# Optimization experiments

Hardware: AMD Instinct MI355X
Metric: run time of the kernel (lower is better)

Reference implementation:

```python
import jax, jax.numpy as jnp
import numpy as np

B, S, D = 2, 2048, 2048
H, DP = 16, 128
WINDOW = 512


def setup_inputs() -> dict:
    key = jax.random.key(0)
    ks = jax.random.split(key, 9)
    sc = 0.02
    return {
        "x": jax.random.normal(ks[0], (B, S, D), dtype=jnp.float32),
        "wq": jax.random.normal(ks[1], (D, H * DP), dtype=jnp.float32) * sc,
        "bq": jax.random.normal(ks[2], (H * DP,), dtype=jnp.float32) * sc,
        "wk": jax.random.normal(ks[3], (D, H * DP), dtype=jnp.float32) * sc,
        "bk": jax.random.normal(ks[4], (H * DP,), dtype=jnp.float32) * sc,
        "wv": jax.random.normal(ks[5], (D, H * DP), dtype=jnp.float32) * sc,
        "bv": jax.random.normal(ks[6], (H * DP,), dtype=jnp.float32) * sc,
        "wo": jax.random.normal(ks[7], (H * DP,), dtype=jnp.float32) * sc,
        "bo": jax.random.normal(ks[8], (1,), dtype=jnp.float32) * sc,
    }


def _sliding_window_mask(seq_len, window):
    q_idx = jnp.arange(seq_len)[:, None]
    kv_idx = jnp.arange(seq_len)[None, :]
    return (q_idx >= kv_idx) & (q_idx - kv_idx < window)


def reference(x, wq, bq, wk, bk, wv, bv, wo, bo):
    b, s, _ = x.shape
    # QKV projections -> (B, H, S, DP)
    q = (x @ wq + bq).reshape(b, s, H, DP).transpose(0, 2, 1, 3)
    k = (x @ wk + bk).reshape(b, s, H, DP).transpose(0, 2, 1, 3)
    v = (x @ wv + bv).reshape(b, s, H, DP).transpose(0, 2, 1, 3)
    scale = 1.0 / np.sqrt(DP).astype(np.float32)
    scores = jnp.einsum("bhqd,bhkd->bhqk", q, k) * scale  # (B,H,S,S)
    mask = _sliding_window_mask(s, WINDOW)
    scores = jnp.where(mask, scores, jnp.finfo(scores.dtype).min)
    attn = jax.nn.softmax(scores, axis=-1)
    o = jnp.einsum("bhqk,bhkd->bhqd", attn, v)  # (B,H,S,DP)
    o = o.transpose(0, 2, 1, 3).reshape(b, s, H * DP)
    return o @ wo + bo[0]  # (B, S)
```

## Files before the change

kernel.cpp:

```cpp
#include <hip/hip_runtime.h>

typedef unsigned short USH;
typedef __bf16 v8bf __attribute__((ext_vector_type(8)));
typedef float v4f __attribute__((ext_vector_type(4)));
typedef unsigned short us8 __attribute__((ext_vector_type(8)));

#define SB 2048
#define DD 2048
#define NH 16
#define DPH 128

__device__ __forceinline__ USH f2bf(float f) {
  unsigned u = __float_as_uint(f);
  u = u + 0x7fffu + ((u >> 16) & 1u);
  return (USH)(u >> 16);
}

#define GL16(gp, lp)                                                   \
  __builtin_amdgcn_global_load_lds(                                    \
      (const __attribute__((address_space(1))) void*)(gp),             \
      (__attribute__((address_space(3))) void*)(lp), 16, 0, 0)

__global__ __launch_bounds__(256) void k_prep(const float* __restrict__ x,
    const float* __restrict__ wq, const float* __restrict__ wk,
    const float* __restrict__ wvf, const float* __restrict__ bvf,
    const float* __restrict__ wo,
    USH* __restrict__ xb, USH* __restrict__ wqt, USH* __restrict__ wkt,
    USH* __restrict__ wvoT, float* __restrict__ bvo, float* __restrict__ out) {
  __shared__ USH tl[64][72];
  __shared__ float red[256];
  const int bid = blockIdx.x;
  const int t = threadIdx.x;
  if (bid < 4096) {
    const int i = (bid * 256 + t) * 8;
    const float4 a = *(const float4*)&x[i];
    const float4 b = *(const float4*)&x[i + 4];
    v8bf o;
    o[0] = (__bf16)a.x; o[1] = (__bf16)a.y; o[2] = (__bf16)a.z; o[3] = (__bf16)a.w;
    o[4] = (__bf16)b.x; o[5] = (__bf16)b.y; o[6] = (__bf16)b.z; o[7] = (__bf16)b.w;
    *(v8bf*)&xb[i] = o;
  } else if (bid < 6144) {
    const int rel = bid - 4096;
    const int z = rel >> 10, rem = rel & 1023;
    const float* w = z ? wk : wq;
    USH* wt = z ? wkt : wqt;
    const int k0 = (rem >> 5) * 64, j0 = (rem & 31) * 64;
#pragma unroll
    for (int p = 0; p < 4; ++p) {
      const int r = p * 16 + (t >> 4);
      const int c = (t & 15) * 4;
      const float4 v = *(const float4*)&w[(size_t)(k0 + r) * DD + j0 + c];
      tl[c + 0][r] = f2bf(v.x);
      tl[c + 1][r] = f2bf(v.y);
      tl[c + 2][r] = f2bf(v.z);
      tl[c + 3][r] = f2bf(v.w);
    }
    __syncthreads();
#pragma unroll
    for (int p = 0; p < 2; ++p) {
      const int j = p * 32 + (t >> 3);
      const int seg = (t & 7) * 8;
      us8 v = *(const us8*)&tl[j][seg];
      *(us8*)&wt[(size_t)(j0 + j) * DD + k0 + seg] = v;
    }
  } else if (bid < 8193) {
    const int d = bid - 6144;
    const float* src = (d == DD) ? bvf : (wvf + (size_t)d * DD);
    const float4 a0 = *(const float4*)&src[t * 8];
    const float4 a1 = *(const float4*)&src[t * 8 + 4];
    const float4 w0 = *(const float4*)&wo[t * 8];
    const float4 w1 = *(const float4*)&wo[t * 8 + 4];
    red[t] = a0.x * w0.x + a0.y * w0.y + a0.z * w0.z + a0.w * w0.w +
             a1.x * w1.x + a1.y * w1.y + a1.z * w1.z + a1.w * w1.w;
    __syncthreads();
    for (int s = 8; s > 0; s >>= 1) {
      if ((t & 15) < s) red[t] += red[t + s];
      __syncthreads();
    }
    if ((t & 15) == 0) {
      if (d == DD) bvo[t >> 4] = red[t];
      else wvoT[(size_t)(t >> 4) * DD + d] = f2bf(red[t]);
    }
  } else {
#pragma unroll
    for (int i = 0; i < 16; ++i) out[i * 256 + t] = 0.f;
  }
}

__global__ __launch_bounds__(64) void k_vw2(const USH* __restrict__ xb,
    const USH* __restrict__ wvoT, const float* __restrict__ bvo,
    float* __restrict__ vw) {
  const int lane = threadIdx.x & 63;
  const int lr = lane & 15, g = lane >> 4;
  const int r0 = blockIdx.x * 16;
  v4f acc = (v4f){0.f, 0.f, 0.f, 0.f};
  const USH* ap = xb + (size_t)(r0 + lr) * DD + g * 8;
  const USH* bp = wvoT + (size_t)lr * DD + g * 8;
#pragma unroll 4
  for (int kt = 0; kt < 64; ++kt) {
    v8bf af = *(const v8bf*)(ap + kt * 32);
    v8bf bf = *(const v8bf*)(bp + kt * 32);
    acc = __builtin_amdgcn_mfma_f32_16x16x32_bf16(af, bf, acc, 0, 0, 0);
  }
  const float bb = bvo[lr];
#pragma unroll
  for (int rr = 0; rr < 4; ++rr) {
    const int row = r0 + g * 4 + rr;
    vw[((size_t)(row >> 11) * NH + lr) * SB + (row & 2047)] = acc[rr] + bb;
  }
}

__global__ __launch_bounds__(512, 2) void k_gemm256(
    const USH* __restrict__ xb,
    const USH* __restrict__ wqt, const USH* __restrict__ wkt,
    const float* __restrict__ bq, const float* __restrict__ bk,
    USH* __restrict__ Qb, USH* __restrict__ Kb) {
  __shared__ USH As[2][16384];
  __shared__ USH Bs[2][16384];
  const int fid = blockIdx.x;
  const int nid = (fid & 7) * 32 + (fid >> 3);
  const int z = nid >> 7;
  const int ty = (nid >> 3) & 15, tx = nid & 7;
  const int row0 = ty * 256, col0 = tx * 256;
  const USH* wt = z ? wkt : wqt;
  const float* bias = z ? bk : bq;
  USH* outp = z ? Kb : Qb;
  const float qscale = z ? 1.0f : 0.08838834764831845f;
  const int t = threadIdx.x;
  const int w = t >> 6, lane = t & 63;
  const int lr = lane & 15, g = lane >> 4;
  const int wr = w >> 2, wc = w & 3;
  size_t gA[4], gB[4];
  int ldsOff[4];
#pragma unroll
  for (int q = 0; q < 4; ++q) {
    const int p = q * 512 + t;
    const int row = p >> 3, ps = p & 7;
    const int sl = ps ^ (row & 7);
    gA[q] = (size_t)(row0 + row) * DD + sl * 8;
    gB[q] = (size_t)(col0 + row) * DD + sl * 8;
    ldsOff[q] = p * 8;
  }
  const int swz = (g ^ (lr & 7)) * 8;
  const int k1o = swz ^ 32;
  const int rowA = wr * 128 + lr;
  const int rowB = wc * 64 + lr;

  v4f acc[8][4];
#pragma unroll
  for (int i = 0; i < 8; ++i)
#pragma unroll
    for (int j = 0; j < 4; ++j) acc[i][j] = (v4f){0.f, 0.f, 0.f, 0.f};

#pragma unroll
  for (int q = 0; q < 4; ++q) {
    GL16(xb + gA[q], &As[0][ldsOff[q]]);
    GL16(wt + gB[q], &Bs[0][ldsOff[q]]);
  }
#pragma unroll
  for (int q = 0; q < 4; ++q) {
    GL16(xb + gA[q] + 64, &As[1][ldsOff[q]]);
    GL16(wt + gB[q] + 64, &Bs[1][ldsOff[q]]);
  }
  asm volatile("s_waitcnt vmcnt(8)" ::: "memory");
  __builtin_amdgcn_s_barrier();
  __builtin_amdgcn_sched_barrier(0);

  v8bf bfr0[4], bfr1[4], af0[4], af4[4], af1[4], af5[4];
#pragma unroll
  for (int ni = 0; ni < 4; ++ni)
    bfr0[ni] = *(const v8bf*)&Bs[0][(rowB + ni * 16) * 64 + swz];
#pragma unroll
  for (int mi = 0; mi < 4; ++mi)
    af0[mi] = *(const v8bf*)&As[0][(rowA + mi * 16) * 64 + swz];

  for (int kt = 0; kt < 32; ++kt) {
    const int c = kt & 1;
    const USH* Ab = &As[c][0];
    const USH* Bb = &Bs[c][0];
    __builtin_amdgcn_sched_barrier(0);
#pragma unroll
    for (int mi = 0; mi < 4; ++mi)
      af4[mi] = *(const v8bf*)&Ab[(rowA + (mi + 4) * 16) * 64 + swz];
    asm volatile("s_waitcnt lgkmcnt(4)" ::: "memory");
    __builtin_amdgcn_sched_barrier(0);
    __builtin_amdgcn_s_setprio(1);
#pragma unroll
    for (int mi = 0; mi < 4; ++mi)
#pragma unroll
      for (int ni = 0; ni < 4; ++ni)
        acc[mi][ni] = __builtin_amdgcn_mfma_f32_16x16x32_bf16(af0[mi], bfr0[ni], acc[mi][ni], 0, 0, 0);
    __builtin_amdgcn_s_setprio(0);
    __builtin_amdgcn_sched_barrier(0);
#pragma unroll
    for (int ni = 0; ni < 4; ++ni)
      bfr1[ni] = *(const v8bf*)&Bb[(rowB + ni * 16) * 64 + k1o];
#pragma unroll
    for (int mi = 0; mi < 4; ++mi)
      af1[mi] = *(const v8bf*)&Ab[(rowA + mi * 16) * 64 + k1o];
    asm volatile("s_waitcnt lgkmcnt(8)" ::: "memory");
    __builtin_amdgcn_sched_barrier(0);
    __builtin_amdgcn_s_setprio(1);
#pragma unroll
    for (int mi = 0; mi < 4; ++mi)
#pragma unroll
      for (int ni = 0; ni < 4; ++ni)
        acc[mi + 4][ni] = __builtin_amdgcn_mfma_f32_16x16x32_bf16(af4[mi], bfr0[ni], acc[mi + 4][ni], 0, 0, 0);
    __builtin_amdgcn_s_setprio(0);
    __builtin_amdgcn_sched_barrier(0);
#pragma unroll
    for (int mi = 0; mi < 4; ++mi)
      af5[mi] = *(const v8bf*)&Ab[(rowA + (mi + 4) * 16) * 64 + k1o];
    asm volatile("s_waitcnt lgkmcnt(4)" ::: "memory");
    __builtin_amdgcn_sched_barrier(0);
    __builtin_amdgcn_s_setprio(1);
#pragma unroll
    for (int mi = 0; mi < 4; ++mi)
#pragma unroll
      for (int ni = 0; ni < 4; ++ni)
        acc[mi][ni] = __builtin_amdgcn_mfma_f32_16x16x32_bf16(af1[mi], bfr1[ni], acc[mi][ni], 0, 0, 0);
    __builtin_amdgcn_s_setprio(0);
    asm volatile("s_waitcnt lgkmcnt(0)" ::: "memory");
    __builtin_amdgcn_sched_barrier(0);
    __builtin_amdgcn_s_barrier();
    if (kt < 30) {
      const size_t ko = (size_t)(kt + 2) * 64;
#pragma unroll
      for (int q = 0; q < 4; ++q) {
        GL16(xb + gA[q] + ko, &As[c][ldsOff[q]]);
        GL16(wt + gB[q] + ko, &Bs[c][ldsOff[q]]);
      }
    }
    __builtin_amdgcn_s_setprio(1);
#pragma unroll
    for (int mi = 0; mi < 4; ++mi)
#pragma unroll
      for (int ni = 0; ni < 4; ++ni)
        acc[mi + 4][ni] = __builtin_amdgcn_mfma_f32_16x16x32_bf16(af5[mi], bfr1[ni], acc[mi + 4][ni], 0, 0, 0);
    __builtin_amdgcn_s_setprio(0);
    if (kt < 31) {
      if (kt < 30) {
        asm volatile("s_waitcnt vmcnt(8)" ::: "memory");
      } else {
        asm volatile("s_waitcnt vmcnt(0)" ::: "memory");
      }
      __builtin_amdgcn_s_barrier();
      __builtin_amdgcn_sched_barrier(0);
      const USH* An = &As[c ^ 1][0];
      const USH* Bn = &Bs[c ^ 1][0];
#pragma unroll
      for (int ni = 0; ni < 4; ++ni)
        bfr0[ni] = *(const v8bf*)&Bn[(rowB + ni * 16) * 64 + swz];
#pragma unroll
      for (int mi = 0; mi < 4; ++mi)
        af0[mi] = *(const v8bf*)&An[(rowA + mi * 16) * 64 + swz];
    }
  }

  {
    const int hh = (col0 + wc * 64) >> 7;
    const int dpb = (wc & 1) * 64;
    float bvv[4];
#pragma unroll
    for (int ni = 0; ni < 4; ++ni)
      bvv[ni] = bias[col0 + wc * 64 + ni * 16 + lr];
#pragma unroll
    for (int mi = 0; mi < 8; ++mi) {
#pragma unroll
      for (int rr = 0; rr < 4; ++rr) {
        const int row = row0 + wr * 128 + mi * 16 + g * 4 + rr;
        const int bi = row >> 11, s = row & 2047;
        USH* op = &outp[(((size_t)bi * NH + hh) * SB + s) * DPH + dpb + lr];
        op[0]  = f2bf((acc[mi][0][rr] + bvv[0]) * qscale);
        op[16] = f2bf((acc[mi][1][rr] + bvv[1]) * qscale);
        op[32] = f2bf((acc[mi][2][rr] + bvv[2]) * qscale);
        op[48] = f2bf((acc[mi][3][rr] + bvv[3]) * qscale);
      }
    }
  }
}

__global__ __launch_bounds__(512) void k_attn(const USH* __restrict__ Qb,
    const USH* __restrict__ Kb, const float* __restrict__ vw,
    const float* __restrict__ bo, float* __restrict__ out) {
  __shared__ USH Ks[2][8192];
  const int bh = blockIdx.y;
  const int t = threadIdx.x;
  const int wid = t >> 6, lane = t & 63;
  const int lr = lane & 15, g = lane >> 4;
  const int qblk = blockIdx.x * 128;
  const int qb = qblk + wid * 16;
  const USH* Qp = Qb + (size_t)bh * SB * DPH;
  const USH* Kp = Kb + (size_t)bh * SB * DPH;
  const float* vwp = vw + (size_t)bh * SB;

  v8bf qf[4];
  {
    const USH* qrp = Qp + (size_t)(qb + lr) * DPH + g * 8;
#pragma unroll
    for (int kc = 0; kc < 4; ++kc) qf[kc] = *(const v8bf*)(qrp + kc * 32);
  }
  size_t srcO[2];
  int ldsO[2];
#pragma unroll
  for (int q = 0; q < 2; ++q) {
    const int r = t >> 3, ps = t & 7;
    srcO[q] = (size_t)r * DPH + q * 64 + (size_t)(((ps ^ (r & 7)) * 8));
    ldsO[q] = (q * 512 + t) * 8;
  }

  float ls[4], os[4];
#pragma unroll
  for (int r = 0; r < 4; ++r) { ls[r] = 0.f; os[r] = 0.f; }

  const int kb0 = qblk > 511 ? qblk - 512 : 0;
  const int kbend = qblk + 64;

  GL16(Kp + (size_t)kb0 * DPH + srcO[0], &Ks[0][ldsO[0]]);
  GL16(Kp + (size_t)kb0 * DPH + srcO[1], &Ks[0][ldsO[1]]);
  __syncthreads();

  int buf = 0;
  for (int kb = kb0; kb <= kbend; kb += 64, buf ^= 1) {
    if (kb < kbend) {
      GL16(Kp + (size_t)(kb + 64) * DPH + srcO[0], &Ks[buf ^ 1][ldsO[0]]);
      GL16(Kp + (size_t)(kb + 64) * DPH + srcO[1], &Ks[buf ^ 1][ldsO[1]]);
    }
    const USH* base = &Ks[buf][0];
    v4f acc[4];
    float vv[4];
#pragma unroll
    for (int i = 0; i < 4; ++i) {
      v4f a = (v4f){0.f, 0.f, 0.f, 0.f};
#pragma unroll
      for (int kc = 0; kc < 4; ++kc) {
        const int lrow = (kc >> 1) * 64 + i * 16 + lr;
        v8bf kf = *(const v8bf*)&base[lrow * 64 + ((((kc & 1) * 4 + g) ^ (lr & 7)) * 8)];
        a = __builtin_amdgcn_mfma_f32_16x16x32_bf16(qf[kc], kf, a, 0, 0, 0);
      }
      acc[i] = a;
      vv[i] = vwp[kb + i * 16 + lr];
    }
#pragma unroll
    for (int r = 0; r < 4; ++r) {
      const int q_i = qb + g * 4 + r;
      const int k0i = kb + lr;
      float sc0 = acc[0][r], sc1 = acc[1][r], sc2 = acc[2][r], sc3 = acc[3][r];
      sc0 = (k0i <= q_i && q_i - k0i < 512) ? sc0 : -1e30f;
      sc1 = (k0i + 16 <= q_i && q_i - (k0i + 16) < 512) ? sc1 : -1e30f;
      sc2 = (k0i + 32 <= q_i && q_i - (k0i + 32) < 512) ? sc2 : -1e30f;
      sc3 = (k0i + 48 <= q_i && q_i - (k0i + 48) < 512) ? sc3 : -1e30f;
      const float p0 = __expf(sc0);
      const float p1 = __expf(sc1);
      const float p2 = __expf(sc2);
      const float p3 = __expf(sc3);
      ls[r] += (p0 + p1) + (p2 + p3);
      os[r] += (p0 * vv[0] + p1 * vv[1]) + (p2 * vv[2] + p3 * vv[3]);
    }
    __syncthreads();
  }
#pragma unroll
  for (int r = 0; r < 4; ++r) {
    os[r] += __shfl_xor(os[r], 1); ls[r] += __shfl_xor(ls[r], 1);
    os[r] += __shfl_xor(os[r], 2); ls[r] += __shfl_xor(ls[r], 2);
    os[r] += __shfl_xor(os[r], 4); ls[r] += __shfl_xor(ls[r], 4);
    os[r] += __shfl_xor(os[r], 8); ls[r] += __shfl_xor(ls[r], 8);
  }
  if (lr == 0) {
    const float bo16 = bo[0] * 0.0625f;
#pragma unroll
    for (int r = 0; r < 4; ++r)
      atomicAdd(&out[(size_t)(bh >> 4) * SB + qb + g * 4 + r], os[r] / ls[r] + bo16);
  }
}

extern "C" void kernel_launch(void* const* d_in, const int* in_sizes, int n_in,
                              void* d_out, int out_size, void* d_ws, size_t ws_size,
                              hipStream_t stream) {
  const float* x   = (const float*)d_in[0];
  const float* wq  = (const float*)d_in[1];
  const float* bq  = (const float*)d_in[2];
  const float* wk  = (const float*)d_in[3];
  const float* bk  = (const float*)d_in[4];
  const float* wvf = (const float*)d_in[5];
  const float* bvf = (const float*)d_in[6];
  const float* wo  = (const float*)d_in[7];
  const float* bo  = (const float*)d_in[8];
  float* out = (float*)d_out;
  char* ws = (char*)d_ws;

  USH*   wqt = (USH*)(ws);
  USH*   wkt = (USH*)(ws + 8388608);
  USH*   Qb  = (USH*)(ws + 16777216);
  USH*   Kb  = (USH*)(ws + 33554432);
  float* vw  = (float*)(ws + 50331648);
  USH*   wvoT= (USH*)(ws + 50593792);
  float* bvo = (float*)(ws + 50724864);
  USH*   xbf = (USH*)(ws + 50987264);

  k_prep<<<dim3(8194), dim3(256), 0, stream>>>(x, wq, wk, wvf, bvf, wo,
                                               xbf, wqt, wkt, wvoT, bvo, out);
  k_vw2<<<dim3(256), dim3(64), 0, stream>>>(xbf, wvoT, bvo, vw);
  k_gemm256<<<dim3(256), dim3(512), 0, stream>>>(xbf, wqt, wkt, bq, bk, Qb, Kb);
  k_attn<<<dim3(16, 32), dim3(512), 0, stream>>>(Qb, Kb, vw, bo, out);
}
```

Measured before the change: 117.0 us.

## Replace 256x256 QK projection GEMM with simpler 128x128 tiled kernel

The Q/K projection GEMM moves from 256x256 tiles with 512 threads and a hand-scheduled, interleaved LDS/MFMA pipeline to 128x128 tiles with 256 threads and a plain double-buffered loop. The launch grows from 256 to 1024 blocks, which gives more blocks per CU and better CU fill. In exchange, each tile reuses its operands less, so more global and LDS traffic is needed per FLOP. It also loses the fine-grained waitcnt and sched_barrier overlap and waits on all loads every iteration.

```diff
diff --git a/kernel.cpp b/kernel.cpp
--- a/kernel.cpp
+++ b/kernel.cpp
@@ -110,18 +110,19 @@
   }
 }
 
-__global__ __launch_bounds__(512, 2) void k_gemm256(
+__global__ __launch_bounds__(256, 2) void k_gemm128(
     const USH* __restrict__ xb,
     const USH* __restrict__ wqt, const USH* __restrict__ wkt,
     const float* __restrict__ bq, const float* __restrict__ bk,
     USH* __restrict__ Qb, USH* __restrict__ Kb) {
-  __shared__ USH As[2][16384];
-  __shared__ USH Bs[2][16384];
+  __shared__ USH As[2][8192];
+  __shared__ USH Bs[2][8192];
   const int fid = blockIdx.x;
-  const int nid = (fid & 7) * 32 + (fid >> 3);
-  const int z = nid >> 7;
-  const int ty = (nid >> 3) & 15, tx = nid & 7;
-  const int row0 = ty * 256, col0 = tx * 256;
+  const int swzid = (fid & 7) * 128 + (fid >> 3);
+  const int z = swzid >> 9;
+  const int rem = swzid & 511;
+  const int ty = rem >> 4, tx = rem & 15;
+  const int row0 = ty * 128, col0 = tx * 128;
   const USH* wt = z ? wkt : wqt;
   const float* bias = z ? bk : bq;
   USH* outp = z ? Kb : Qb;
@@ -129,12 +130,12 @@
   const int t = threadIdx.x;
   const int w = t >> 6, lane = t & 63;
   const int lr = lane & 15, g = lane >> 4;
-  const int wr = w >> 2, wc = w & 3;
+  const int wr = w >> 1, wc = w & 1;
   size_t gA[4], gB[4];
   int ldsOff[4];
 #pragma unroll
   for (int q = 0; q < 4; ++q) {
-    const int p = q * 512 + t;
+    const int p = q * 256 + t;
     const int row = p >> 3, ps = p & 7;
     const int sl = ps ^ (row & 7);
     gA[q] = (size_t)(row0 + row) * DD + sl * 8;
@@ -142,13 +143,12 @@
     ldsOff[q] = p * 8;
   }
   const int swz = (g ^ (lr & 7)) * 8;
-  const int k1o = swz ^ 32;
-  const int rowA = wr * 128 + lr;
+  const int rowA = wr * 64 + lr;
   const int rowB = wc * 64 + lr;
 
-  v4f acc[8][4];
-#pragma unroll
-  for (int i = 0; i < 8; ++i)
+  v4f acc[4][4];
+#pragma unroll
+  for (int i = 0; i < 4; ++i)
 #pragma unroll
     for (int j = 0; j < 4; ++j) acc[i][j] = (v4f){0.f, 0.f, 0.f, 0.f};
 
@@ -157,118 +157,53 @@
     GL16(xb + gA[q], &As[0][ldsOff[q]]);
     GL16(wt + gB[q], &Bs[0][ldsOff[q]]);
   }
-#pragma unroll
-  for (int q = 0; q < 4; ++q) {
-    GL16(xb + gA[q] + 64, &As[1][ldsOff[q]]);
-    GL16(wt + gB[q] + 64, &Bs[1][ldsOff[q]]);
-  }
-  asm volatile("s_waitcnt vmcnt(8)" ::: "memory");
-  __builtin_amdgcn_s_barrier();
-  __builtin_amdgcn_sched_barrier(0);
-
-  v8bf bfr0[4], bfr1[4], af0[4], af4[4], af1[4], af5[4];
-#pragma unroll
-  for (int ni = 0; ni < 4; ++ni)
-    bfr0[ni] = *(const v8bf*)&Bs[0][(rowB + ni * 16) * 64 + swz];
-#pragma unroll
-  for (int mi = 0; mi < 4; ++mi)
-    af0[mi] = *(const v8bf*)&As[0][(rowA + mi * 16) * 64 + swz];
+  asm volatile("s_waitcnt vmcnt(0)" ::: "memory");
+  __syncthreads();
 
   for (int kt = 0; kt < 32; ++kt) {
     const int c = kt & 1;
-    const USH* Ab = &As[c][0];
-    const USH* Bb = &Bs[c][0];
-    __builtin_amdgcn_sched_barrier(0);
-#pragma unroll
-    for (int mi = 0; mi < 4; ++mi)
-      af4[mi] = *(const v8bf*)&Ab[(rowA + (mi + 4) * 16) * 64 + swz];
-    asm volatile("s_waitcnt lgkmcnt(4)" ::: "memory");
-    __builtin_amdgcn_sched_barrier(0);
-    __builtin_amdgcn_s_setprio(1);
-#pragma unroll
-    for (int mi = 0; mi < 4; ++mi)
+    if (kt < 31) {
+      const size_t ko = (size_t)(kt + 1) * 64;
+#pragma unroll
+      for (int q = 0; q < 4; ++q) {
+        GL16(xb + gA[q] + ko, &As[c ^ 1][ldsOff[q]]);
+        GL16(wt + gB[q] + ko, &Bs[c ^ 1][ldsOff[q]]);
+      }
+    }
+#pragma unroll
+    for (int ka = 0; ka < 2; ++ka) {
+      const int kx = swz ^ (ka * 32);
+      v8bf af[4], bfr[4];
 #pragma unroll
       for (int ni = 0; ni < 4; ++ni)
-        acc[mi][ni] = __builtin_amdgcn_mfma_f32_16x16x32_bf16(af0[mi], bfr0[ni], acc[mi][ni], 0, 0, 0);
-    __builtin_amdgcn_s_setprio(0);
-    __builtin_amdgcn_sched_barrier(0);
-#pragma unroll
-    for (int ni = 0; ni < 4; ++ni)
-      bfr1[ni] = *(const v8bf*)&Bb[(rowB + ni * 16) * 64 + k1o];
-#pragma unroll
-    for (int mi = 0; mi < 4; ++mi)
-      af1[mi] = *(const v8bf*)&Ab[(rowA + mi * 16) * 64 + k1o];
-    asm volatile("s_waitcnt lgkmcnt(8)" ::: "memory");
-    __builtin_amdgcn_sched_barrier(0);
-    __builtin_amdgcn_s_setprio(1);
-#pragma unroll
-    for (int mi = 0; mi < 4; ++mi)
-#pragma unroll
-      for (int ni = 0; ni < 4; ++ni)
-        acc[mi + 4][ni] = __builtin_amdgcn_mfma_f32_16x16x32_bf16(af4[mi], bfr0[ni], acc[mi + 4][ni], 0, 0, 0);
-    __builtin_amdgcn_s_setprio(0);
-    __builtin_amdgcn_sched_barrier(0);
-#pragma unroll
-    for (int mi = 0; mi < 4; ++mi)
-      af5[mi] = *(const v8bf*)&Ab[(rowA + (mi + 4) * 16) * 64 + k1o];
-    asm volatile("s_waitcnt lgkmcnt(4)" ::: "memory");
-    __builtin_amdgcn_sched_barrier(0);
-    __builtin_amdgcn_s_setprio(1);
-#pragma unroll
-    for (int mi = 0; mi < 4; ++mi)
-#pragma unroll
-      for (int ni = 0; ni < 4; ++ni)
-        acc[mi][ni] = __builtin_amdgcn_mfma_f32_16x16x32_bf16(af1[mi], bfr1[ni], acc[mi][ni], 0, 0, 0);
-    __builtin_amdgcn_s_setprio(0);
-    asm volatile("s_waitcnt lgkmcnt(0)" ::: "memory");
-    __builtin_amdgcn_sched_barrier(0);
-    __builtin_amdgcn_s_barrier();
-    if (kt < 30) {
-      const size_t ko = (size_t)(kt + 2) * 64;
-#pragma unroll
-      for (int q = 0; q < 4; ++q) {
-        GL16(xb + gA[q] + ko, &As[c][ldsOff[q]]);
-        GL16(wt + gB[q] + ko, &Bs[c][ldsOff[q]]);
-      }
-    }
-    __builtin_amdgcn_s_setprio(1);
-#pragma unroll
-    for (int mi = 0; mi < 4; ++mi)
-#pragma unroll
-      for (int ni = 0; ni < 4; ++ni)
-        acc[mi + 4][ni] = __builtin_amdgcn_mfma_f32_16x16x32_bf16(af5[mi], bfr1[ni], acc[mi + 4][ni], 0, 0, 0);
-    __builtin_amdgcn_s_setprio(0);
-    if (kt < 31) {
-      if (kt < 30) {
-        asm volatile("s_waitcnt vmcnt(8)" ::: "memory");
-      } else {
-        asm volatile("s_waitcnt vmcnt(0)" ::: "memory");
-      }
-      __builtin_amdgcn_s_barrier();
-      __builtin_amdgcn_sched_barrier(0);
-      const USH* An = &As[c ^ 1][0];
-      const USH* Bn = &Bs[c ^ 1][0];
-#pragma unroll
-      for (int ni = 0; ni < 4; ++ni)
-        bfr0[ni] = *(const v8bf*)&Bn[(rowB + ni * 16) * 64 + swz];
+        bfr[ni] = *(const v8bf*)&Bs[c][(rowB + ni * 16) * 64 + kx];
 #pragma unroll
       for (int mi = 0; mi < 4; ++mi)
-        af0[mi] = *(const v8bf*)&An[(rowA + mi * 16) * 64 + swz];
-    }
+        af[mi] = *(const v8bf*)&As[c][(rowA + mi * 16) * 64 + kx];
+      __builtin_amdgcn_s_setprio(1);
+#pragma unroll
+      for (int mi = 0; mi < 4; ++mi)
+#pragma unroll
+        for (int ni = 0; ni < 4; ++ni)
+          acc[mi][ni] = __builtin_amdgcn_mfma_f32_16x16x32_bf16(af[mi], bfr[ni], acc[mi][ni], 0, 0, 0);
+      __builtin_amdgcn_s_setprio(0);
+    }
+    asm volatile("s_waitcnt vmcnt(0)" ::: "memory");
+    __syncthreads();
   }
 
   {
     const int hh = (col0 + wc * 64) >> 7;
-    const int dpb = (wc & 1) * 64;
+    const int dpb = (col0 + wc * 64) & 127;
     float bvv[4];
 #pragma unroll
     for (int ni = 0; ni < 4; ++ni)
       bvv[ni] = bias[col0 + wc * 64 + ni * 16 + lr];
 #pragma unroll
-    for (int mi = 0; mi < 8; ++mi) {
+    for (int mi = 0; mi < 4; ++mi) {
 #pragma unroll
       for (int rr = 0; rr < 4; ++rr) {
-        const int row = row0 + wr * 128 + mi * 16 + g * 4 + rr;
+        const int row = row0 + wr * 64 + mi * 16 + g * 4 + rr;
         const int bi = row >> 11, s = row & 2047;
         USH* op = &outp[(((size_t)bi * NH + hh) * SB + s) * DPH + dpb + lr];
         op[0]  = f2bf((acc[mi][0][rr] + bvv[0]) * qscale);
@@ -401,6 +336,6 @@
   k_prep<<<dim3(8194), dim3(256), 0, stream>>>(x, wq, wk, wvf, bvf, wo,
                                                xbf, wqt, wkt, wvoT, bvo, out);
   k_vw2<<<dim3(256), dim3(64), 0, stream>>>(xbf, wvoT, bvo, vw);
-  k_gemm256<<<dim3(256), dim3(512), 0, stream>>>(xbf, wqt, wkt, bq, bk, Qb, Kb);
+  k_gemm128<<<dim3(1024), dim3(256), 0, stream>>>(xbf, wqt, wkt, bq, bk, Qb, Kb);
   k_attn<<<dim3(16, 32), dim3(512), 0, stream>>>(Qb, Kb, vw, bo, out);
 }
```

Measured after the change: 127.2 us. +8.8%, slower.
